# Kernel optimization log

Hardware: AMD Instinct MI355X
Metric: run time of the kernel (lower is better)

## Reference

```python
import jax, jax.numpy as jnp
import numpy as np

H = 256

def setup_inputs() -> dict:
    key = jax.random.key(0)
    ks = jax.random.split(key, 8)
    B, S = 32, 4096
    hidden = jax.random.normal(ks[0], (B, H), dtype=jnp.float32)
    encoder_outputs = jax.random.normal(ks[1], (B, S, H), dtype=jnp.float32)
    scale = 1.0 / np.sqrt(H)
    W1_w = jax.random.uniform(ks[2], (H, H), jnp.float32, -scale, scale)
    W1_b = jax.random.uniform(ks[3], (H,), jnp.float32, -scale, scale)
    W2_w = jax.random.uniform(ks[4], (H, H), jnp.float32, -scale, scale)
    W2_b = jax.random.uniform(ks[5], (H,), jnp.float32, -scale, scale)
    V_w = jax.random.uniform(ks[6], (H, 1), jnp.float32, -scale, scale)
    V_b = jax.random.uniform(ks[7], (1,), jnp.float32, -scale, scale)
    return {"hidden": hidden, "encoder_outputs": encoder_outputs,
            "W1_w": W1_w, "W1_b": W1_b, "W2_w": W2_w, "W2_b": W2_b,
            "V_w": V_w, "V_b": V_b}

def reference(hidden, encoder_outputs, W1_w, W1_b, W2_w, W2_b, V_w, V_b):
    # hidden: (B,H), encoder_outputs: (B,S,H)
    q = hidden @ W1_w + W1_b                     # (B,H)
    k = jnp.einsum('bsh,hd->bsd', encoder_outputs, W2_w) + W2_b  # (B,S,H)
    energy = jnp.tanh(q[:, None, :] + k)         # (B,S,H)
    scores = jnp.einsum('bsh,ho->bso', energy, V_w) + V_b        # (B,S,1)
    attention_weights = jax.nn.softmax(scores, axis=1)           # (B,S,1)
    context_vector = jnp.einsum('bso,bsh->bh', attention_weights, encoder_outputs)  # (B,H)
    return attention_weights, context_vector
```

## Files before the change

### kernel.cpp

```cpp
#include <hip/hip_runtime.h>
#include <hip/hip_bf16.h>
#include <math.h>

#define BB 32
#define SS 4096
#define HH 256

typedef __bf16 bf16x8 __attribute__((ext_vector_type(8)));
typedef float f32x4 __attribute__((ext_vector_type(4)));

__device__ inline bf16x8 cvt8(const float4& x, const float4& y) {
    union { __hip_bfloat162 p[4]; bf16x8 v; } u;
    u.p[0] = __float22bfloat162_rn(make_float2(x.x, x.y));
    u.p[1] = __float22bfloat162_rn(make_float2(x.z, x.w));
    u.p[2] = __float22bfloat162_rn(make_float2(y.x, y.y));
    u.p[3] = __float22bfloat162_rn(make_float2(y.z, y.w));
    return u.v;
}

__device__ inline float fast_tanh(float x) {
    float xc = fminf(fmaxf(x, -10.f), 10.f);
    float e  = __expf(2.f * xc);
    return (e - 1.f) * __builtin_amdgcn_rcpf(e + 1.f);
}

__global__ void prep_kernel(const float* __restrict__ W2_w,
                            ushort* __restrict__ w2sw,
                            const float* __restrict__ hidden,
                            const float* __restrict__ W1_w,
                            const float* __restrict__ W1_b,
                            const float* __restrict__ W2_b,
                            const float* __restrict__ V_w,
                            float* __restrict__ qq,
                            float* __restrict__ Mout) {
    __shared__ float red[HH];
    const int t = threadIdx.x;
    if (blockIdx.x < 256) {
        const int i = blockIdx.x * 256 + t;
        const int j    = i & 7;
        const int lane = (i >> 3) & 63;
        const int nt   = (i >> 9) & 15;
        const int kc   = i >> 13;
        const int k = kc * 32 + ((lane >> 4) & 3) * 8 + j;
        const int n = nt * 16 + (lane & 15);
        __hip_bfloat16 h = __float2bfloat16(W2_w[k * HH + n]);
        w2sw[i] = *(ushort*)&h;
    } else if (blockIdx.x < 256 + BB) {
        const int b = blockIdx.x - 256;
        red[t] = hidden[b * HH + t];
        __syncthreads();
        float acc = 0.f;
#pragma unroll 16
        for (int k = 0; k < HH; ++k)
            acc = fmaf(red[k], W1_w[k * HH + t], acc);
        qq[b * HH + t] = acc + W1_b[t] + W2_b[t];
    } else {
        red[t] = fabsf(V_w[t]);
        __syncthreads();
        for (int off = 128; off > 0; off >>= 1) {
            if (t < off) red[t] += red[t + off];
            __syncthreads();
        }
        if (t == 0) Mout[0] = red[0];
    }
}

__global__ __launch_bounds__(256, 2)
void score_ctx_kernel(const float* __restrict__ enc,
                      const ushort* __restrict__ w2sw,
                      const float* __restrict__ qq,
                      const float* __restrict__ V_w,
                      const float* __restrict__ Mptr,
                      float* __restrict__ wtilde_out,
                      float* __restrict__ part) {
    __shared__ float sc_lds[64];
    __shared__ float accl[4][HH];

    const int t    = threadIdx.x;
    const int b    = blockIdx.y;
    const int c    = blockIdx.x;
    const int s0   = c * 64;
    const int wave = t >> 6;
    const int lane = t & 63;
    const int mw   = wave & 1;
    const int nw   = wave >> 1;
    const int l15  = lane & 15;
    const int quad = lane >> 4;

    f32x4 acc[2][8];
#pragma unroll
    for (int mt = 0; mt < 2; ++mt)
#pragma unroll
        for (int nt = 0; nt < 8; ++nt) acc[mt][nt] = (f32x4)0.f;

    const bf16x8* bgl = (const bf16x8*)w2sw + (size_t)(nw * 8) * 64 + lane;
    const float* aptr0 =
        enc + ((size_t)(b * SS + s0 + mw * 32 + l15)) * HH + quad * 8;
    const float* aptr1 = aptr0 + (size_t)16 * HH;

    bf16x8 bq[2][8];
    float4 ax[2][2], ay[2][2];

#pragma unroll
    for (int nt = 0; nt < 8; ++nt) bq[0][nt] = bgl[nt * 64];
    ax[0][0] = *(const float4*)aptr0;
    ay[0][0] = *(const float4*)(aptr0 + 4);
    ax[0][1] = *(const float4*)aptr1;
    ay[0][1] = *(const float4*)(aptr1 + 4);

#pragma unroll
    for (int kc = 0; kc < 8; ++kc) {
        const int cur = kc & 1;
        if (kc < 7) {
#pragma unroll
            for (int nt = 0; nt < 8; ++nt)
                bq[cur ^ 1][nt] = bgl[(kc + 1) * 1024 + nt * 64];
            const int o = (kc + 1) * 32;
            ax[cur ^ 1][0] = *(const float4*)(aptr0 + o);
            ay[cur ^ 1][0] = *(const float4*)(aptr0 + o + 4);
            ax[cur ^ 1][1] = *(const float4*)(aptr1 + o);
            ay[cur ^ 1][1] = *(const float4*)(aptr1 + o + 4);
        }
        bf16x8 af0 = cvt8(ax[cur][0], ay[cur][0]);
        bf16x8 af1 = cvt8(ax[cur][1], ay[cur][1]);
#pragma unroll
        for (int nt = 0; nt < 8; ++nt) {
            acc[0][nt] = __builtin_amdgcn_mfma_f32_16x16x32_bf16(
                af0, bq[cur][nt], acc[0][nt], 0, 0, 0);
            acc[1][nt] = __builtin_amdgcn_mfma_f32_16x16x32_bf16(
                af1, bq[cur][nt], acc[1][nt], 0, 0, 0);
        }
    }

    float p[2][4] = {{0.f, 0.f, 0.f, 0.f}, {0.f, 0.f, 0.f, 0.f}};
#pragma unroll
    for (int nt = 0; nt < 8; ++nt) {
        const int n = nw * 128 + nt * 16 + l15;
        const float qn = qq[b * HH + n];
        const float vn = V_w[n];
#pragma unroll
        for (int mt = 0; mt < 2; ++mt)
#pragma unroll
            for (int r = 0; r < 4; ++r)
                p[mt][r] = fmaf(vn, fast_tanh(qn + acc[mt][nt][r]), p[mt][r]);
    }
#pragma unroll
    for (int off = 1; off < 16; off <<= 1)
#pragma unroll
        for (int mt = 0; mt < 2; ++mt)
#pragma unroll
            for (int r = 0; r < 4; ++r)
                p[mt][r] += __shfl_xor(p[mt][r], off);

    if (nw == 0 && l15 == 0) {
#pragma unroll
        for (int mt = 0; mt < 2; ++mt)
            *(float4*)&sc_lds[mw * 32 + mt * 16 + quad * 4] =
                make_float4(p[mt][0], p[mt][1], p[mt][2], p[mt][3]);
    }
    __syncthreads();
    const float Mv = Mptr[0];
    if (nw == 1 && l15 == 0) {
#pragma unroll
        for (int mt = 0; mt < 2; ++mt) {
            const int row = mw * 32 + mt * 16 + quad * 4;
            float4 h = *(const float4*)&sc_lds[row];
            float4 v = make_float4(__expf(h.x + p[mt][0] - Mv),
                                   __expf(h.y + p[mt][1] - Mv),
                                   __expf(h.z + p[mt][2] - Mv),
                                   __expf(h.w + p[mt][3] - Mv));
            *(float4*)&sc_lds[row] = v;
            *(float4*)&wtilde_out[b * SS + s0 + row] = v;
        }
    }
    __syncthreads();

    const int tr = t >> 6;
    const int h0 = (t & 63) * 4;
    float4 a = make_float4(0.f, 0.f, 0.f, 0.f);
    const float* ep = enc + ((size_t)(b * SS + s0)) * HH;
#pragma unroll
    for (int jj = 0; jj < 16; ++jj) {
        const int j = jj * 4 + tr;
        const float4 e = *(const float4*)(ep + (size_t)j * HH + h0);
        const float w = sc_lds[j];
        a.x = fmaf(w, e.x, a.x);
        a.y = fmaf(w, e.y, a.y);
        a.z = fmaf(w, e.z, a.z);
        a.w = fmaf(w, e.w, a.w);
    }
    *(float4*)&accl[tr][h0] = a;
    __syncthreads();

    part[((size_t)(b * 64 + c)) * HH + t] =
        accl[0][t] + accl[1][t] + accl[2][t] + accl[3][t];
}

__global__ __launch_bounds__(256)
void finish_kernel(const float* __restrict__ part,
                   float* __restrict__ weights_out,
                   float* __restrict__ ctx_out) {
    __shared__ float red[256];
    __shared__ float linv_s;
    const int b = blockIdx.x;
    const int t = threadIdx.x;

    float4* wo4 = (float4*)(weights_out + (size_t)b * SS);
    float4 vals[4];
    float l = 0.f;
#pragma unroll
    for (int i = 0; i < 4; ++i) {
        vals[i] = wo4[i * 256 + t];
        l += vals[i].x + vals[i].y + vals[i].z + vals[i].w;
    }
    red[t] = l;
    __syncthreads();
    for (int off = 128; off > 0; off >>= 1) {
        if (t < off) red[t] += red[t + off];
        __syncthreads();
    }
    if (t == 0) linv_s = 1.f / red[0];
    __syncthreads();
    const float linv = linv_s;

#pragma unroll
    for (int i = 0; i < 4; ++i) {
        const float4 v = vals[i];
        wo4[i * 256 + t] =
            make_float4(v.x * linv, v.y * linv, v.z * linv, v.w * linv);
    }

    float a = 0.f;
#pragma unroll 8
    for (int c = 0; c < 64; ++c)
        a += part[((size_t)(b * 64 + c)) * HH + t];
    ctx_out[b * HH + t] = a * linv;
}

extern "C" void kernel_launch(void* const* d_in, const int* in_sizes, int n_in,
                              void* d_out, int out_size, void* d_ws, size_t ws_size,
                              hipStream_t stream) {
    const float* hidden = (const float*)d_in[0];
    const float* enc    = (const float*)d_in[1];
    const float* W1_w   = (const float*)d_in[2];
    const float* W1_b   = (const float*)d_in[3];
    const float* W2_w   = (const float*)d_in[4];
    const float* W2_b   = (const float*)d_in[5];
    const float* V_w    = (const float*)d_in[6];
    const float* V_b    = (const float*)d_in[7];
    (void)V_b;

    float* out_weights = (float*)d_out;
    float* out_ctx     = (float*)d_out + BB * SS;

    float* ws      = (float*)d_ws;
    float* ws_qq   = ws;
    float* ws_part = ws_qq + BB * HH;
    float* ws_M    = ws_part + BB * 64 * HH;
    ushort* ws_w2  = (ushort*)(ws_M + 4);

    prep_kernel<<<dim3(256 + BB + 1), dim3(256), 0, stream>>>(
        W2_w, ws_w2, hidden, W1_w, W1_b, W2_b, V_w, ws_qq, ws_M);
    score_ctx_kernel<<<dim3(SS / 64, BB), dim3(256), 0, stream>>>(
        enc, ws_w2, ws_qq, V_w, ws_M, out_weights, ws_part);
    finish_kernel<<<dim3(BB), dim3(256), 0, stream>>>(
        ws_part, out_weights, out_ctx);
}
```

Measured before the change: 253.3 us.

## Make score kernel persistent over four tiles with cross-tile A prefetch

Result: slower. 322.4 us (+27.3%).

```diff
diff --git a/kernel.cpp b/kernel.cpp
--- a/kernel.cpp
+++ b/kernel.cpp
@@ -77,9 +77,6 @@
     __shared__ float accl[4][HH];
 
     const int t    = threadIdx.x;
-    const int b    = blockIdx.y;
-    const int c    = blockIdx.x;
-    const int s0   = c * 64;
     const int wave = t >> 6;
     const int lane = t & 63;
     const int mw   = wave & 1;
@@ -87,113 +84,146 @@
     const int l15  = lane & 15;
     const int quad = lane >> 4;
 
-    f32x4 acc[2][8];
-#pragma unroll
-    for (int mt = 0; mt < 2; ++mt)
-#pragma unroll
-        for (int nt = 0; nt < 8; ++nt) acc[mt][nt] = (f32x4)0.f;
+    const int tile0 = blockIdx.x * 4;
+    const int b     = tile0 >> 6;
 
     const bf16x8* bgl = (const bf16x8*)w2sw + (size_t)(nw * 8) * 64 + lane;
-    const float* aptr0 =
-        enc + ((size_t)(b * SS + s0 + mw * 32 + l15)) * HH + quad * 8;
-    const float* aptr1 = aptr0 + (size_t)16 * HH;
-
-    bf16x8 bq[2][8];
-    float4 ax[2][2], ay[2][2];
-
-#pragma unroll
-    for (int nt = 0; nt < 8; ++nt) bq[0][nt] = bgl[nt * 64];
-    ax[0][0] = *(const float4*)aptr0;
-    ay[0][0] = *(const float4*)(aptr0 + 4);
-    ax[0][1] = *(const float4*)aptr1;
-    ay[0][1] = *(const float4*)(aptr1 + 4);
-
-#pragma unroll
-    for (int kc = 0; kc < 8; ++kc) {
-        const int cur = kc & 1;
-        if (kc < 7) {
-#pragma unroll
-            for (int nt = 0; nt < 8; ++nt)
-                bq[cur ^ 1][nt] = bgl[(kc + 1) * 1024 + nt * 64];
-            const int o = (kc + 1) * 32;
-            ax[cur ^ 1][0] = *(const float4*)(aptr0 + o);
-            ay[cur ^ 1][0] = *(const float4*)(aptr0 + o + 4);
-            ax[cur ^ 1][1] = *(const float4*)(aptr1 + o);
-            ay[cur ^ 1][1] = *(const float4*)(aptr1 + o + 4);
-        }
-        bf16x8 af0 = cvt8(ax[cur][0], ay[cur][0]);
-        bf16x8 af1 = cvt8(ax[cur][1], ay[cur][1]);
-#pragma unroll
-        for (int nt = 0; nt < 8; ++nt) {
-            acc[0][nt] = __builtin_amdgcn_mfma_f32_16x16x32_bf16(
-                af0, bq[cur][nt], acc[0][nt], 0, 0, 0);
-            acc[1][nt] = __builtin_amdgcn_mfma_f32_16x16x32_bf16(
-                af1, bq[cur][nt], acc[1][nt], 0, 0, 0);
-        }
-    }
-
-    float p[2][4] = {{0.f, 0.f, 0.f, 0.f}, {0.f, 0.f, 0.f, 0.f}};
+
+    const float Mv = Mptr[0];
+    float qv[8], vv[8];
 #pragma unroll
     for (int nt = 0; nt < 8; ++nt) {
         const int n = nw * 128 + nt * 16 + l15;
-        const float qn = qq[b * HH + n];
-        const float vn = V_w[n];
+        qv[nt] = qq[b * HH + n];
+        vv[nt] = V_w[n];
+    }
+
+    auto abase = [&](int tile) -> const float* {
+        const int c = tile & 63;
+        return enc + ((size_t)(b * SS + c * 64 + mw * 32 + l15)) * HH + quad * 8;
+    };
+
+    bf16x8 bq[2][8];
+    float4 ax[4][2], ay[4][2];
+
+    const float* aptr = abase(tile0);
+#pragma unroll
+    for (int nt = 0; nt < 8; ++nt) bq[0][nt] = bgl[nt * 64];
+#pragma unroll
+    for (int s = 0; s < 2; ++s)
+#pragma unroll
+        for (int mt = 0; mt < 2; ++mt) {
+            const float* p = aptr + (size_t)mt * 16 * HH + s * 32;
+            ax[s][mt] = *(const float4*)p;
+            ay[s][mt] = *(const float4*)(p + 4);
+        }
+
+    for (int tt = 0; tt < 4; ++tt) {
+        const int tile = tile0 + tt;
+        const int c    = tile & 63;
+        const int s0   = c * 64;
+        const float* aptrN = abase(tt < 3 ? tile + 1 : tile0);
+
+        f32x4 acc[2][8];
 #pragma unroll
         for (int mt = 0; mt < 2; ++mt)
 #pragma unroll
-            for (int r = 0; r < 4; ++r)
-                p[mt][r] = fmaf(vn, fast_tanh(qn + acc[mt][nt][r]), p[mt][r]);
-    }
-#pragma unroll
-    for (int off = 1; off < 16; off <<= 1)
-#pragma unroll
-        for (int mt = 0; mt < 2; ++mt)
-#pragma unroll
-            for (int r = 0; r < 4; ++r)
-                p[mt][r] += __shfl_xor(p[mt][r], off);
-
-    if (nw == 0 && l15 == 0) {
-#pragma unroll
-        for (int mt = 0; mt < 2; ++mt)
-            *(float4*)&sc_lds[mw * 32 + mt * 16 + quad * 4] =
-                make_float4(p[mt][0], p[mt][1], p[mt][2], p[mt][3]);
-    }
-    __syncthreads();
-    const float Mv = Mptr[0];
-    if (nw == 1 && l15 == 0) {
-#pragma unroll
-        for (int mt = 0; mt < 2; ++mt) {
-            const int row = mw * 32 + mt * 16 + quad * 4;
-            float4 h = *(const float4*)&sc_lds[row];
-            float4 v = make_float4(__expf(h.x + p[mt][0] - Mv),
-                                   __expf(h.y + p[mt][1] - Mv),
-                                   __expf(h.z + p[mt][2] - Mv),
-                                   __expf(h.w + p[mt][3] - Mv));
-            *(float4*)&sc_lds[row] = v;
-            *(float4*)&wtilde_out[b * SS + s0 + row] = v;
-        }
-    }
-    __syncthreads();
-
-    const int tr = t >> 6;
-    const int h0 = (t & 63) * 4;
-    float4 a = make_float4(0.f, 0.f, 0.f, 0.f);
-    const float* ep = enc + ((size_t)(b * SS + s0)) * HH;
-#pragma unroll
-    for (int jj = 0; jj < 16; ++jj) {
-        const int j = jj * 4 + tr;
-        const float4 e = *(const float4*)(ep + (size_t)j * HH + h0);
-        const float w = sc_lds[j];
-        a.x = fmaf(w, e.x, a.x);
-        a.y = fmaf(w, e.y, a.y);
-        a.z = fmaf(w, e.z, a.z);
-        a.w = fmaf(w, e.w, a.w);
-    }
-    *(float4*)&accl[tr][h0] = a;
-    __syncthreads();
-
-    part[((size_t)(b * 64 + c)) * HH + t] =
-        accl[0][t] + accl[1][t] + accl[2][t] + accl[3][t];
+            for (int nt = 0; nt < 8; ++nt) acc[mt][nt] = (f32x4)0.f;
+
+#pragma unroll
+        for (int kc = 0; kc < 8; ++kc) {
+            {
+                const int p = (kc + 1) & 7;
+#pragma unroll
+                for (int nt = 0; nt < 8; ++nt)
+                    bq[(kc + 1) & 1][nt] = bgl[p * 1024 + nt * 64];
+            }
+            {
+                const int slot = (kc + 2) & 3;
+                const float* pb = (kc < 6) ? (aptr + (kc + 2) * 32)
+                                           : (aptrN + (kc - 6) * 32);
+#pragma unroll
+                for (int mt = 0; mt < 2; ++mt) {
+                    const float* p = pb + (size_t)mt * 16 * HH;
+                    ax[slot][mt] = *(const float4*)p;
+                    ay[slot][mt] = *(const float4*)(p + 4);
+                }
+            }
+            asm volatile("" ::: "memory");
+
+            const int cs = kc & 3, cb = kc & 1;
+            bf16x8 af0 = cvt8(ax[cs][0], ay[cs][0]);
+            bf16x8 af1 = cvt8(ax[cs][1], ay[cs][1]);
+#pragma unroll
+            for (int nt = 0; nt < 8; ++nt) {
+                acc[0][nt] = __builtin_amdgcn_mfma_f32_16x16x32_bf16(
+                    af0, bq[cb][nt], acc[0][nt], 0, 0, 0);
+                acc[1][nt] = __builtin_amdgcn_mfma_f32_16x16x32_bf16(
+                    af1, bq[cb][nt], acc[1][nt], 0, 0, 0);
+            }
+        }
+        aptr = aptrN;
+
+        float p[2][4] = {{0.f, 0.f, 0.f, 0.f}, {0.f, 0.f, 0.f, 0.f}};
+#pragma unroll
+        for (int nt = 0; nt < 8; ++nt) {
+#pragma unroll
+            for (int mt = 0; mt < 2; ++mt)
+#pragma unroll
+                for (int r = 0; r < 4; ++r)
+                    p[mt][r] = fmaf(vv[nt], fast_tanh(qv[nt] + acc[mt][nt][r]),
+                                    p[mt][r]);
+        }
+#pragma unroll
+        for (int off = 1; off < 16; off <<= 1)
+#pragma unroll
+            for (int mt = 0; mt < 2; ++mt)
+#pragma unroll
+                for (int r = 0; r < 4; ++r)
+                    p[mt][r] += __shfl_xor(p[mt][r], off);
+
+        if (nw == 0 && l15 == 0) {
+#pragma unroll
+            for (int mt = 0; mt < 2; ++mt)
+                *(float4*)&sc_lds[mw * 32 + mt * 16 + quad * 4] =
+                    make_float4(p[mt][0], p[mt][1], p[mt][2], p[mt][3]);
+        }
+        __syncthreads();
+        if (nw == 1 && l15 == 0) {
+#pragma unroll
+            for (int mt = 0; mt < 2; ++mt) {
+                const int row = mw * 32 + mt * 16 + quad * 4;
+                float4 h = *(const float4*)&sc_lds[row];
+                float4 v = make_float4(__expf(h.x + p[mt][0] - Mv),
+                                       __expf(h.y + p[mt][1] - Mv),
+                                       __expf(h.z + p[mt][2] - Mv),
+                                       __expf(h.w + p[mt][3] - Mv));
+                *(float4*)&sc_lds[row] = v;
+                *(float4*)&wtilde_out[b * SS + s0 + row] = v;
+            }
+        }
+        __syncthreads();
+
+        const int tr = t >> 6;
+        const int h0 = (t & 63) * 4;
+        float4 a = make_float4(0.f, 0.f, 0.f, 0.f);
+        const float* ep = enc + ((size_t)(b * SS + s0)) * HH;
+#pragma unroll
+        for (int jj = 0; jj < 16; ++jj) {
+            const int j = jj * 4 + tr;
+            const float4 e = *(const float4*)(ep + (size_t)j * HH + h0);
+            const float w = sc_lds[j];
+            a.x = fmaf(w, e.x, a.x);
+            a.y = fmaf(w, e.y, a.y);
+            a.z = fmaf(w, e.z, a.z);
+            a.w = fmaf(w, e.w, a.w);
+        }
+        *(float4*)&accl[tr][h0] = a;
+        __syncthreads();
+
+        part[((size_t)(b * 64 + c)) * HH + t] =
+            accl[0][t] + accl[1][t] + accl[2][t] + accl[3][t];
+    }
 }
 
 __global__ __launch_bounds__(256)
@@ -261,7 +291,7 @@
 
     prep_kernel<<<dim3(256 + BB + 1), dim3(256), 0, stream>>>(
         W2_w, ws_w2, hidden, W1_w, W1_b, W2_b, V_w, ws_qq, ws_M);
-    score_ctx_kernel<<<dim3(SS / 64, BB), dim3(256), 0, stream>>>(
+    score_ctx_kernel<<<dim3(512), dim3(256), 0, stream>>>(
         enc, ws_w2, ws_qq, V_w, ws_M, out_weights, ws_part);
     finish_kernel<<<dim3(BB), dim3(256), 0, stream>>>(
         ws_part, out_weights, out_ctx);
```

## Stage encoder tiles into LDS with async double-buffered loads in persistent blocks

Applied to the files above, without the earlier changes.

New measurement: 316.5 us. 24.9% more time.

```diff
diff --git a/kernel.cpp b/kernel.cpp
--- a/kernel.cpp
+++ b/kernel.cpp
@@ -8,6 +8,9 @@
 
 typedef __bf16 bf16x8 __attribute__((ext_vector_type(8)));
 typedef float f32x4 __attribute__((ext_vector_type(4)));
+
+#define GLOBAL_AS __attribute__((address_space(1)))
+#define LDS_AS    __attribute__((address_space(3)))
 
 __device__ inline bf16x8 cvt8(const float4& x, const float4& y) {
     union { __hip_bfloat162 p[4]; bf16x8 v; } u;
@@ -65,7 +68,7 @@
     }
 }
 
-__global__ __launch_bounds__(256, 2)
+__global__ __launch_bounds__(512, 2)
 void score_ctx_kernel(const float* __restrict__ enc,
                       const ushort* __restrict__ w2sw,
                       const float* __restrict__ qq,
@@ -73,127 +76,141 @@
                       const float* __restrict__ Mptr,
                       float* __restrict__ wtilde_out,
                       float* __restrict__ part) {
-    __shared__ float sc_lds[64];
-    __shared__ float accl[4][HH];
+    __shared__ float Abuf[2][16384];
+    __shared__ float sc_part[4][64];
+    __shared__ float sc_w[64];
+    __shared__ float accl2[2][HH];
 
     const int t    = threadIdx.x;
-    const int b    = blockIdx.y;
-    const int c    = blockIdx.x;
-    const int s0   = c * 64;
     const int wave = t >> 6;
     const int lane = t & 63;
     const int mw   = wave & 1;
-    const int nw   = wave >> 1;
+    const int nh   = wave >> 1;
     const int l15  = lane & 15;
     const int quad = lane >> 4;
-
-    f32x4 acc[2][8];
-#pragma unroll
-    for (int mt = 0; mt < 2; ++mt)
-#pragma unroll
-        for (int nt = 0; nt < 8; ++nt) acc[mt][nt] = (f32x4)0.f;
-
-    const bf16x8* bgl = (const bf16x8*)w2sw + (size_t)(nw * 8) * 64 + lane;
-    const float* aptr0 =
-        enc + ((size_t)(b * SS + s0 + mw * 32 + l15)) * HH + quad * 8;
-    const float* aptr1 = aptr0 + (size_t)16 * HH;
-
-    bf16x8 bq[2][8];
-    float4 ax[2][2], ay[2][2];
-
-#pragma unroll
-    for (int nt = 0; nt < 8; ++nt) bq[0][nt] = bgl[nt * 64];
-    ax[0][0] = *(const float4*)aptr0;
-    ay[0][0] = *(const float4*)(aptr0 + 4);
-    ax[0][1] = *(const float4*)aptr1;
-    ay[0][1] = *(const float4*)(aptr1 + 4);
-
-#pragma unroll
-    for (int kc = 0; kc < 8; ++kc) {
-        const int cur = kc & 1;
-        if (kc < 7) {
-#pragma unroll
-            for (int nt = 0; nt < 8; ++nt)
-                bq[cur ^ 1][nt] = bgl[(kc + 1) * 1024 + nt * 64];
-            const int o = (kc + 1) * 32;
-            ax[cur ^ 1][0] = *(const float4*)(aptr0 + o);
-            ay[cur ^ 1][0] = *(const float4*)(aptr0 + o + 4);
-            ax[cur ^ 1][1] = *(const float4*)(aptr1 + o);
-            ay[cur ^ 1][1] = *(const float4*)(aptr1 + o + 4);
-        }
-        bf16x8 af0 = cvt8(ax[cur][0], ay[cur][0]);
-        bf16x8 af1 = cvt8(ax[cur][1], ay[cur][1]);
-#pragma unroll
-        for (int nt = 0; nt < 8; ++nt) {
-            acc[0][nt] = __builtin_amdgcn_mfma_f32_16x16x32_bf16(
-                af0, bq[cur][nt], acc[0][nt], 0, 0, 0);
-            acc[1][nt] = __builtin_amdgcn_mfma_f32_16x16x32_bf16(
-                af1, bq[cur][nt], acc[1][nt], 0, 0, 0);
-        }
-    }
-
-    float p[2][4] = {{0.f, 0.f, 0.f, 0.f}, {0.f, 0.f, 0.f, 0.f}};
-#pragma unroll
-    for (int nt = 0; nt < 8; ++nt) {
-        const int n = nw * 128 + nt * 16 + l15;
-        const float qn = qq[b * HH + n];
-        const float vn = V_w[n];
+    const int b    = blockIdx.y;
+    const int seg  = blockIdx.x;
+
+    const bf16x8* bgl = (const bf16x8*)w2sw;
+    bf16x8 bq[8][4];
+#pragma unroll
+    for (int kc = 0; kc < 8; ++kc)
+#pragma unroll
+        for (int nt = 0; nt < 4; ++nt)
+            bq[kc][nt] = bgl[kc * 1024 + (nh * 4 + nt) * 64 + lane];
+
+    const float Mv = Mptr[0];
+    float qv[4], vv[4];
+#pragma unroll
+    for (int nt = 0; nt < 4; ++nt) {
+        const int n = (nh * 4 + nt) * 16 + l15;
+        qv[nt] = qq[b * HH + n];
+        vv[nt] = V_w[n];
+    }
+
+    auto stage = [&](int c, int bufi) {
+        const char* gbase = (const char*)(enc + ((size_t)(b * SS + c * 64)) * HH);
+        char* lbase = (char*)&Abuf[bufi][0];
+#pragma unroll
+        for (int i = 0; i < 8; ++i) {
+            const int s  = i * 512 + t;
+            const int r  = s >> 6;
+            const int cp = s & 63;
+            const int g  = r * 64 + ((cp & 56) | ((cp & 7) ^ (r & 7)));
+            __builtin_amdgcn_global_load_lds(
+                (const GLOBAL_AS void*)(gbase + (size_t)g * 16),
+                (LDS_AS void*)(lbase + i * 8192 + wave * 1024), 16, 0, 0);
+        }
+    };
+
+    stage(seg * 8, 0);
+
+    for (int ii = 0; ii < 8; ++ii) {
+        const int cur = ii & 1;
+        const int c   = seg * 8 + ii;
+        const int s0  = c * 64;
+        __syncthreads();
+
+        f32x4 acc[2][4];
 #pragma unroll
         for (int mt = 0; mt < 2; ++mt)
 #pragma unroll
-            for (int r = 0; r < 4; ++r)
-                p[mt][r] = fmaf(vn, fast_tanh(qn + acc[mt][nt][r]), p[mt][r]);
-    }
-#pragma unroll
-    for (int off = 1; off < 16; off <<= 1)
-#pragma unroll
-        for (int mt = 0; mt < 2; ++mt)
-#pragma unroll
-            for (int r = 0; r < 4; ++r)
-                p[mt][r] += __shfl_xor(p[mt][r], off);
-
-    if (nw == 0 && l15 == 0) {
-#pragma unroll
-        for (int mt = 0; mt < 2; ++mt)
-            *(float4*)&sc_lds[mw * 32 + mt * 16 + quad * 4] =
-                make_float4(p[mt][0], p[mt][1], p[mt][2], p[mt][3]);
-    }
-    __syncthreads();
-    const float Mv = Mptr[0];
-    if (nw == 1 && l15 == 0) {
-#pragma unroll
-        for (int mt = 0; mt < 2; ++mt) {
-            const int row = mw * 32 + mt * 16 + quad * 4;
-            float4 h = *(const float4*)&sc_lds[row];
-            float4 v = make_float4(__expf(h.x + p[mt][0] - Mv),
-                                   __expf(h.y + p[mt][1] - Mv),
-                                   __expf(h.z + p[mt][2] - Mv),
-                                   __expf(h.w + p[mt][3] - Mv));
-            *(float4*)&sc_lds[row] = v;
-            *(float4*)&wtilde_out[b * SS + s0 + row] = v;
-        }
-    }
-    __syncthreads();
-
-    const int tr = t >> 6;
-    const int h0 = (t & 63) * 4;
-    float4 a = make_float4(0.f, 0.f, 0.f, 0.f);
-    const float* ep = enc + ((size_t)(b * SS + s0)) * HH;
-#pragma unroll
-    for (int jj = 0; jj < 16; ++jj) {
-        const int j = jj * 4 + tr;
-        const float4 e = *(const float4*)(ep + (size_t)j * HH + h0);
-        const float w = sc_lds[j];
-        a.x = fmaf(w, e.x, a.x);
-        a.y = fmaf(w, e.y, a.y);
-        a.z = fmaf(w, e.z, a.z);
-        a.w = fmaf(w, e.w, a.w);
-    }
-    *(float4*)&accl[tr][h0] = a;
-    __syncthreads();
-
-    part[((size_t)(b * 64 + c)) * HH + t] =
-        accl[0][t] + accl[1][t] + accl[2][t] + accl[3][t];
+            for (int nt = 0; nt < 4; ++nt) acc[mt][nt] = (f32x4)0.f;
+
+#pragma unroll
+        for (int kc = 0; kc < 8; ++kc) {
+            bf16x8 af[2];
+#pragma unroll
+            for (int mt = 0; mt < 2; ++mt) {
+                const int R  = mw * 32 + mt * 16 + l15;
+                const int c0 = kc * 8 + quad * 2;
+                const int x0 = (c0 & 56) | ((c0 & 7) ^ (R & 7));
+                const int x1 = (c0 & 56) | (((c0 + 1) & 7) ^ (R & 7));
+                const float4 x = *(const float4*)&Abuf[cur][(R * 64 + x0) * 4];
+                const float4 y = *(const float4*)&Abuf[cur][(R * 64 + x1) * 4];
+                af[mt] = cvt8(x, y);
+            }
+#pragma unroll
+            for (int nt = 0; nt < 4; ++nt) {
+                acc[0][nt] = __builtin_amdgcn_mfma_f32_16x16x32_bf16(
+                    af[0], bq[kc][nt], acc[0][nt], 0, 0, 0);
+                acc[1][nt] = __builtin_amdgcn_mfma_f32_16x16x32_bf16(
+                    af[1], bq[kc][nt], acc[1][nt], 0, 0, 0);
+            }
+        }
+
+        if (ii < 7) stage(c + 1, cur ^ 1);
+
+        float p[2][4] = {{0.f, 0.f, 0.f, 0.f}, {0.f, 0.f, 0.f, 0.f}};
+#pragma unroll
+        for (int nt = 0; nt < 4; ++nt)
+#pragma unroll
+            for (int mt = 0; mt < 2; ++mt)
+#pragma unroll
+                for (int r = 0; r < 4; ++r)
+                    p[mt][r] = fmaf(vv[nt], fast_tanh(qv[nt] + acc[mt][nt][r]),
+                                    p[mt][r]);
+#pragma unroll
+        for (int off = 1; off < 16; off <<= 1)
+#pragma unroll
+            for (int mt = 0; mt < 2; ++mt)
+#pragma unroll
+                for (int r = 0; r < 4; ++r)
+                    p[mt][r] += __shfl_xor(p[mt][r], off);
+
+        if (l15 == 0) {
+#pragma unroll
+            for (int mt = 0; mt < 2; ++mt)
+                *(float4*)&sc_part[nh][mw * 32 + mt * 16 + quad * 4] =
+                    make_float4(p[mt][0], p[mt][1], p[mt][2], p[mt][3]);
+        }
+        __syncthreads();
+        if (t < 64) {
+            const float s = sc_part[0][t] + sc_part[1][t] +
+                            sc_part[2][t] + sc_part[3][t];
+            const float wt = __expf(s - Mv);
+            sc_w[t] = wt;
+            wtilde_out[b * SS + s0 + t] = wt;
+        }
+        __syncthreads();
+
+        {
+            const int h  = t & 255;
+            const int jg = t >> 8;
+            const int ch = h >> 2, hr = h & 3;
+            float a = 0.f;
+#pragma unroll
+            for (int jj = 0; jj < 32; ++jj) {
+                const int j  = jj * 2 + jg;
+                const int cs = (ch & 56) | ((ch & 7) ^ (j & 7));
+                a = fmaf(sc_w[j], Abuf[cur][(j * 64 + cs) * 4 + hr], a);
+            }
+            accl2[jg][h] = a;
+        }
+        __syncthreads();
+        if (t < HH)
+            part[((size_t)(b * 64 + c)) * HH + t] = accl2[0][t] + accl2[1][t];
+    }
 }
 
 __global__ __launch_bounds__(256)
@@ -261,7 +278,7 @@
 
     prep_kernel<<<dim3(256 + BB + 1), dim3(256), 0, stream>>>(
         W2_w, ws_w2, hidden, W1_w, W1_b, W2_b, V_w, ws_qq, ws_M);
-    score_ctx_kernel<<<dim3(SS / 64, BB), dim3(256), 0, stream>>>(
+    score_ctx_kernel<<<dim3(8, BB), dim3(512), 0, stream>>>(
         enc, ws_w2, ws_qq, V_w, ws_M, out_weights, ws_part);
     finish_kernel<<<dim3(BB), dim3(256), 0, stream>>>(
         ws_part, out_weights, out_ctx);
```
